# Optimization experiments

Measured on AMD Instinct MI355X. Metric: run time of the kernel, lower is better.

The kernel has to match this reference:

```python
import jax, jax.numpy as jnp
import numpy as np


def setup_inputs() -> dict:
    key = jax.random.key(0)
    ks = jax.random.split(key, 8)
    B, C, H, W = 4, 128, 64, 64
    d = C // 8
    return {
        "x": jax.random.normal(ks[0], (B, C, H, W), dtype=jnp.float32),
        "wq": jax.random.normal(ks[1], (d, C), dtype=jnp.float32) * 0.05,
        "bq": jax.random.normal(ks[2], (d,), dtype=jnp.float32) * 0.05,
        "wk": jax.random.normal(ks[3], (d, C), dtype=jnp.float32) * 0.05,
        "bk": jax.random.normal(ks[4], (d,), dtype=jnp.float32) * 0.05,
        "wv": jax.random.normal(ks[5], (C, C), dtype=jnp.float32) * 0.05,
        "bv": jax.random.normal(ks[6], (C,), dtype=jnp.float32) * 0.05,
        "gamma": jax.random.normal(ks[7], (1,), dtype=jnp.float32),
    }


def reference(x, wq, bq, wk, bk, wv, bv, gamma):
    B, C, H, W = x.shape
    N = H * W
    xf = x.reshape(B, C, N)                                  # [B,C,N]
    # 1x1 convs == per-pixel linear projections
    q = jnp.einsum('bcn,dc->bdn', xf, wq) + bq[None, :, None]  # [B,d,N]
    k = jnp.einsum('bcn,dc->bdn', xf, wk) + bk[None, :, None]  # [B,d,N]
    v = jnp.einsum('bcn,oc->bon', xf, wv) + bv[None, :, None]  # [B,C,N]
    scale = jnp.asarray(C, x.dtype) ** 0.5                     # note: scaled by sqrt(C), per source
    scores = jnp.einsum('bdn,bdm->bnm', q, k) / scale          # [B,N,N]
    attn = jax.nn.softmax(scores, axis=2)
    out = jnp.einsum('bcm,bnm->bcn', v, attn).reshape(B, C, H, W)
    return gamma[0] * out + x
```

## Files before the change

kernel.cpp:

```cpp
#include <hip/hip_runtime.h>
#include <hip/hip_bf16.h>
#include <math.h>

#define NB 4
#define NC 128
#define NN 4096
#define ND 16

typedef short s16x8 __attribute__((ext_vector_type(8)));
typedef float f32x4 __attribute__((ext_vector_type(4)));
typedef unsigned int u32;

extern "C" __device__ float __ocml_native_exp2_f32(float);

__device__ __forceinline__ unsigned short f2b(float f) {
    __hip_bfloat16 h = __float2bfloat16(f);
    return *reinterpret_cast<unsigned short*>(&h);
}
__device__ __forceinline__ u32 f2b2(float lo, float hi) {
    __hip_bfloat162 h2 = __float22bfloat162_rn(make_float2(lo, hi));
    return *reinterpret_cast<u32*>(&h2);
}
__device__ __forceinline__ void gll16(const unsigned short* src, unsigned short* ldsdst) {
    __builtin_amdgcn_global_load_lds((const __attribute__((address_space(1))) u32*)src,
                                     (__attribute__((address_space(3))) u32*)ldsdst, 16, 0, 0);
}

__global__ __launch_bounds__(256) void proj_kernel(
    const float* __restrict__ x,
    const float* __restrict__ wq, const float* __restrict__ bq,
    const float* __restrict__ wk, const float* __restrict__ bk,
    const float* __restrict__ wv, const float* __restrict__ bv,
    unsigned short* __restrict__ Qb, unsigned short* __restrict__ Kb,
    unsigned short* __restrict__ Vt)
{
    __shared__ unsigned short xsw[64 * 128];
    __shared__ unsigned short wsw[160 * 128];
    __shared__ float bl[160];

    const int t  = threadIdx.x;
    const int b  = blockIdx.x >> 6;
    const int n0 = (blockIdx.x & 63) << 6;

#pragma unroll
    for (int p = 0; p < 8; ++p) {
        const int idx = (p * 256 + t) * 4;
        const int c = idx >> 6, px0 = idx & 63;
        const float4 v4 = *(const float4*)&x[((size_t)(b * NC + c)) * NN + n0 + px0];
#pragma unroll
        for (int j = 0; j < 4; ++j) {
            const int px = px0 + j;
            xsw[px * 128 + (((c >> 3) ^ (px & 15)) << 3) + (c & 7)] = f2b((&v4.x)[j]);
        }
    }
#pragma unroll
    for (int p = 0; p < 20; ++p) {
        const int idx = (p * 256 + t) * 4;
        const int o = idx >> 7, c0 = idx & 127;
        const float* src = (o < 16) ? (wq + o * NC)
                         : (o < 32) ? (wk + (o - 16) * NC)
                                    : (wv + (o - 32) * NC);
        const float4 v4 = *(const float4*)&src[c0];
#pragma unroll
        for (int j = 0; j < 4; ++j) {
            const int c = c0 + j;
            wsw[o * 128 + (((c >> 3) ^ (o & 15)) << 3) + (c & 7)] = f2b((&v4.x)[j]);
        }
    }
    if (t < 160) bl[t] = (t < 16) ? bq[t] : (t < 32) ? bk[t - 16] : bv[t - 32];
    __syncthreads();

    const int lane = t & 63, w = t >> 6;
    const int l = lane & 15, h = lane >> 4;
    const int pxt = w;

    s16x8 af[4];
#pragma unroll
    for (int ks = 0; ks < 4; ++ks) {
        const int px = pxt * 16 + l;
        af[ks] = *(const s16x8*)&xsw[px * 128 + ((((ks * 4) + h) ^ (px & 15)) << 3)];
    }

    const float qscale = 1.4426950408889634f / sqrtf(128.0f);

#pragma unroll
    for (int ot = 0; ot < 10; ++ot) {
        f32x4 acc = (f32x4){0.f, 0.f, 0.f, 0.f};
        const int o = ot * 16 + l;
#pragma unroll
        for (int ks = 0; ks < 4; ++ks) {
            const s16x8 bf = *(const s16x8*)&wsw[o * 128 + ((((ks * 4) + h) ^ l) << 3)];
            acc = __builtin_amdgcn_mfma_f32_16x16x32_bf16(af[ks], bf, acc, 0, 0, 0);
        }
        const float bias = bl[o];
        if (ot == 0) {
#pragma unroll
            for (int r = 0; r < 4; ++r) {
                const int px = pxt * 16 + h * 4 + r;
                Qb[((size_t)b * NN + n0 + px) * ND + l] = f2b((acc[r] + bias) * qscale);
            }
        } else if (ot == 1) {
#pragma unroll
            for (int r = 0; r < 4; ++r) {
                const int px = pxt * 16 + h * 4 + r;
                Kb[((size_t)b * NN + n0 + px) * ND + l] = f2b(acc[r] + bias);
            }
        } else {
            const int c = ot * 16 + l - 32;
            uint2 pk;
            pk.x = f2b2(acc[0] + bias, acc[1] + bias);
            pk.y = f2b2(acc[2] + bias, acc[3] + bias);
            const int px0 = pxt * 16 + h * 4;
            *(uint2*)&Vt[((size_t)b * NC + c) * NN + n0 + px0] = pk;
        }
    }
}

__global__ __launch_bounds__(256) void attn_kernel(
    const unsigned short* __restrict__ Qb, const unsigned short* __restrict__ Kb,
    const unsigned short* __restrict__ Vt, const float* __restrict__ x,
    const float* __restrict__ gammap, float* __restrict__ out)
{
    __shared__ unsigned short vsw[2][128 * 64];
    __shared__ unsigned short ksh[2][64 * 24];
    __shared__ unsigned short psw[4][16 * 64];

    const int t    = threadIdx.x;
    const int lane = t & 63, w = t >> 6;
    const int l = lane & 15, h = lane >> 4;
    const int nt = w >> 1, ch = w & 1;

    const int bid = blockIdx.x;
    const int r_ = bid >> 8, s_ = bid & 255, xcd = s_ & 7, cu = s_ >> 3;
    const int b = xcd >> 1;
    const int tile = cu + ((xcd & 1) << 5) + (r_ << 6);
    const int n0 = tile << 5;

    s16x8 qf = {0, 0, 0, 0, 0, 0, 0, 0};
    if (h < 2) qf = *(const s16x8*)&Qb[((size_t)b * NN + n0 + nt * 16 + l) * ND + h * 8];

    const int vch = (lane & 7) ^ (lane >> 3);
    const int km = t >> 2, kp = t & 3;

    float mrun = -1e30f, lrun = 0.0f;
    f32x4 acc[4];
#pragma unroll
    for (int ct = 0; ct < 4; ++ct) acc[ct] = (f32x4){0.f, 0.f, 0.f, 0.f};

#pragma unroll
    for (int i = 0; i < 4; ++i) {
        const int c = w * 32 + i * 8 + (lane >> 3);
        gll16(&Vt[((size_t)b * NC + c) * NN + 0 + vch * 8],
              (unsigned short*)((char*)&vsw[0][0] + w * 4096 + i * 1024));
    }
    uint2 kreg = *(const uint2*)&Kb[((size_t)b * NN + 0 + km) * ND + kp * 4];
    *(uint2*)&ksh[0][km * 24 + kp * 4] = kreg;
    kreg = *(const uint2*)&Kb[((size_t)b * NN + 64 + km) * ND + kp * 4];
    __syncthreads();

    int cur = 0;
    for (int it = 0; it < 64; ++it) {
        const int m0n = ((it + 1) & 63) << 6;
#pragma unroll
        for (int i = 0; i < 4; ++i) {
            const int c = w * 32 + i * 8 + (lane >> 3);
            gll16(&Vt[((size_t)b * NC + c) * NN + m0n + vch * 8],
                  (unsigned short*)((char*)&vsw[cur ^ 1][0] + w * 4096 + i * 1024));
        }
        *(uint2*)&ksh[cur ^ 1][km * 24 + kp * 4] = kreg;
        kreg = *(const uint2*)&Kb[((size_t)b * NN + (((it + 2) & 63) << 6) + km) * ND + kp * 4];

        f32x4 sacc[4];
#pragma unroll
        for (int mt = 0; mt < 4; ++mt) {
            s16x8 afk = {0, 0, 0, 0, 0, 0, 0, 0};
            if (h < 2) afk = *(const s16x8*)&ksh[cur][(mt * 16 + l) * 24 + h * 8];
            sacc[mt] = __builtin_amdgcn_mfma_f32_16x16x32_bf16(
                afk, qf, (f32x4){0.f, 0.f, 0.f, 0.f}, 0, 0, 0);
        }

        float pmax = sacc[0][0];
#pragma unroll
        for (int mt = 0; mt < 4; ++mt)
#pragma unroll
            for (int r = 0; r < 4; ++r) pmax = fmaxf(pmax, sacc[mt][r]);
        pmax = fmaxf(pmax, __shfl_xor(pmax, 16));
        pmax = fmaxf(pmax, __shfl_xor(pmax, 32));
        const float mnew = fmaxf(mrun, pmax);
        const float rr = __ocml_native_exp2_f32(mrun - mnew);

        float p[4][4];
        float lsum = 0.0f;
#pragma unroll
        for (int mt = 0; mt < 4; ++mt)
#pragma unroll
            for (int r = 0; r < 4; ++r) {
                p[mt][r] = __ocml_native_exp2_f32(sacc[mt][r] - mnew);
                lsum += p[mt][r];
            }
        lsum += __shfl_xor(lsum, 16);
        lsum += __shfl_xor(lsum, 32);
        lrun = lrun * rr + lsum;
        mrun = mnew;

#pragma unroll
        for (int ct = 0; ct < 4; ++ct)
#pragma unroll
            for (int r = 0; r < 4; ++r) acc[ct][r] *= rr;

#pragma unroll
        for (int mt = 0; mt < 4; ++mt) {
            const int mch = mt * 2 + (h >> 1);
            const int base = l * 64 + ((mch ^ (l & 7)) << 3) + ((h & 1) << 2);
            *(u32*)&psw[w][base]     = f2b2(p[mt][0], p[mt][1]);
            *(u32*)&psw[w][base + 2] = f2b2(p[mt][2], p[mt][3]);
        }
        s16x8 pf[2];
#pragma unroll
        for (int kb = 0; kb < 2; ++kb)
            pf[kb] = *(const s16x8*)&psw[w][l * 64 + (((kb * 4 + h) ^ (l & 7)) << 3)];

#pragma unroll
        for (int ct = 0; ct < 4; ++ct) {
            const int c = ch * 64 + ct * 16 + l;
#pragma unroll
            for (int kb = 0; kb < 2; ++kb) {
                const s16x8 vf = *(const s16x8*)&vsw[cur][c * 64 + ((((kb * 4) + h) ^ (c & 7)) << 3)];
                acc[ct] = __builtin_amdgcn_mfma_f32_16x16x32_bf16(vf, pf[kb], acc[ct], 0, 0, 0);
            }
        }
        __syncthreads();
        cur ^= 1;
    }

    const float g = gammap[0];
    const float linv = 1.0f / lrun;
    const int n = n0 + nt * 16 + l;
#pragma unroll
    for (int ct = 0; ct < 4; ++ct)
#pragma unroll
        for (int r = 0; r < 4; ++r) {
            const int c = ch * 64 + ct * 16 + h * 4 + r;
            const size_t idx = ((size_t)b * NC + c) * NN + n;
            out[idx] = g * (acc[ct][r] * linv) + x[idx];
        }
}

extern "C" void kernel_launch(void* const* d_in, const int* in_sizes, int n_in,
                              void* d_out, int out_size, void* d_ws, size_t ws_size,
                              hipStream_t stream)
{
    const float* x  = (const float*)d_in[0];
    const float* wq = (const float*)d_in[1];
    const float* bq = (const float*)d_in[2];
    const float* wk = (const float*)d_in[3];
    const float* bk = (const float*)d_in[4];
    const float* wv = (const float*)d_in[5];
    const float* bv = (const float*)d_in[6];
    const float* gm = (const float*)d_in[7];
    float* out = (float*)d_out;

    unsigned short* Qb = (unsigned short*)d_ws;
    unsigned short* Kb = Qb + (size_t)NB * NN * ND;
    unsigned short* Vt = Kb + (size_t)NB * NN * ND;

    hipLaunchKernelGGL(proj_kernel, dim3(NB * 64), dim3(256), 0, stream,
                       x, wq, bq, wk, bk, wv, bv, Qb, Kb, Vt);
    hipLaunchKernelGGL(attn_kernel, dim3(512), dim3(256), 0, stream,
                       Qb, Kb, Vt, x, gm, out);
}
```

Before: 156.9 us.

## Rewrite attention with 32x32 MFMA, split-KV waves and LDS-free streaming

Adds a prep kernel that converts the weights to bf16 and folds the softmax scale into wq/bq. The projection kernel now reads x straight into registers, and V is stored in a 16-column tiled layout. The attention kernel moves to 32x32x16 MFMA and splits the KV range across wave pairs, merging their partial results through LDS at the end. Inside the loop it drops the LDS staging of K, V and P and passes P between lanes with shuffles instead. The goals are to cut LDS traffic and sync barriers and to raise MFMA efficiency, at the cost of uncoalesced direct global loads and an extra kernel launch.

```diff
diff --git a/kernel.cpp b/kernel.cpp
--- a/kernel.cpp
+++ b/kernel.cpp
@@ -5,10 +5,10 @@
 #define NB 4
 #define NC 128
 #define NN 4096
-#define ND 16
 
 typedef short s16x8 __attribute__((ext_vector_type(8)));
 typedef float f32x4 __attribute__((ext_vector_type(4)));
+typedef float f32x16 __attribute__((ext_vector_type(16)));
 typedef unsigned int u32;
 
 extern "C" __device__ float __ocml_native_exp2_f32(float);
@@ -21,229 +21,215 @@
     __hip_bfloat162 h2 = __float22bfloat162_rn(make_float2(lo, hi));
     return *reinterpret_cast<u32*>(&h2);
 }
-__device__ __forceinline__ void gll16(const unsigned short* src, unsigned short* ldsdst) {
-    __builtin_amdgcn_global_load_lds((const __attribute__((address_space(1))) u32*)src,
-                                     (__attribute__((address_space(3))) u32*)ldsdst, 16, 0, 0);
-}
-
-__global__ __launch_bounds__(256) void proj_kernel(
-    const float* __restrict__ x,
+
+__global__ __launch_bounds__(256) void prep_kernel(
     const float* __restrict__ wq, const float* __restrict__ bq,
     const float* __restrict__ wk, const float* __restrict__ bk,
     const float* __restrict__ wv, const float* __restrict__ bv,
+    unsigned short* __restrict__ Wb, float* __restrict__ Bf)
+{
+    const float s = 1.4426950408889634f / sqrtf(128.0f);
+    const int idx = blockIdx.x * 256 + threadIdx.x;
+    const int o = idx >> 7, c = idx & 127;
+    float v;
+    if (o < 16)      v = wq[o * 128 + c] * s;
+    else if (o < 32) v = wk[(o - 16) * 128 + c];
+    else             v = wv[(o - 32) * 128 + c];
+    Wb[o * 128 + c] = f2b(v);
+    if (blockIdx.x == 0 && threadIdx.x < 160) {
+        const int oo = threadIdx.x;
+        Bf[oo] = (oo < 16) ? bq[oo] * s : (oo < 32) ? bk[oo - 16] : bv[oo - 32];
+    }
+}
+
+__global__ __launch_bounds__(256, 2) void proj_kernel(
+    const float* __restrict__ x, const unsigned short* __restrict__ Wb,
+    const float* __restrict__ Bf,
     unsigned short* __restrict__ Qb, unsigned short* __restrict__ Kb,
-    unsigned short* __restrict__ Vt)
-{
-    __shared__ unsigned short xsw[64 * 128];
-    __shared__ unsigned short wsw[160 * 128];
-    __shared__ float bl[160];
-
-    const int t  = threadIdx.x;
-    const int b  = blockIdx.x >> 6;
-    const int n0 = (blockIdx.x & 63) << 6;
-
-#pragma unroll
-    for (int p = 0; p < 8; ++p) {
-        const int idx = (p * 256 + t) * 4;
-        const int c = idx >> 6, px0 = idx & 63;
-        const float4 v4 = *(const float4*)&x[((size_t)(b * NC + c)) * NN + n0 + px0];
-#pragma unroll
-        for (int j = 0; j < 4; ++j) {
-            const int px = px0 + j;
-            xsw[px * 128 + (((c >> 3) ^ (px & 15)) << 3) + (c & 7)] = f2b((&v4.x)[j]);
-        }
-    }
-#pragma unroll
-    for (int p = 0; p < 20; ++p) {
-        const int idx = (p * 256 + t) * 4;
-        const int o = idx >> 7, c0 = idx & 127;
-        const float* src = (o < 16) ? (wq + o * NC)
-                         : (o < 32) ? (wk + (o - 16) * NC)
-                                    : (wv + (o - 32) * NC);
-        const float4 v4 = *(const float4*)&src[c0];
-#pragma unroll
-        for (int j = 0; j < 4; ++j) {
-            const int c = c0 + j;
-            wsw[o * 128 + (((c >> 3) ^ (o & 15)) << 3) + (c & 7)] = f2b((&v4.x)[j]);
-        }
-    }
-    if (t < 160) bl[t] = (t < 16) ? bq[t] : (t < 32) ? bk[t - 16] : bv[t - 32];
-    __syncthreads();
-
+    unsigned short* __restrict__ V2)
+{
+    const int t = threadIdx.x;
     const int lane = t & 63, w = t >> 6;
     const int l = lane & 15, h = lane >> 4;
-    const int pxt = w;
-
-    s16x8 af[4];
+    const int pxt = w & 1, oh = w >> 1;
+    const int b = blockIdx.x >> 7;
+    const int n0 = (blockIdx.x & 127) * 32;
+    const int n = n0 + pxt * 16 + l;
+
+    s16x8 bx[4];
 #pragma unroll
     for (int ks = 0; ks < 4; ++ks) {
-        const int px = pxt * 16 + l;
-        af[ks] = *(const s16x8*)&xsw[px * 128 + ((((ks * 4) + h) ^ (px & 15)) << 3)];
-    }
-
-    const float qscale = 1.4426950408889634f / sqrtf(128.0f);
-
-#pragma unroll
-    for (int ot = 0; ot < 10; ++ot) {
+        float xv[8];
+#pragma unroll
+        for (int j = 0; j < 8; ++j)
+            xv[j] = x[((size_t)(b * 128 + ks * 32 + h * 8 + j)) * 4096 + n];
+        u32* pw = (u32*)&bx[ks];
+        pw[0] = f2b2(xv[0], xv[1]);
+        pw[1] = f2b2(xv[2], xv[3]);
+        pw[2] = f2b2(xv[4], xv[5]);
+        pw[3] = f2b2(xv[6], xv[7]);
+    }
+
+#pragma unroll
+    for (int i = 0; i < 5; ++i) {
+        const int ot = oh * 5 + i;
+        const int o0 = ot * 16;
         f32x4 acc = (f32x4){0.f, 0.f, 0.f, 0.f};
-        const int o = ot * 16 + l;
 #pragma unroll
         for (int ks = 0; ks < 4; ++ks) {
-            const s16x8 bf = *(const s16x8*)&wsw[o * 128 + ((((ks * 4) + h) ^ l) << 3)];
-            acc = __builtin_amdgcn_mfma_f32_16x16x32_bf16(af[ks], bf, acc, 0, 0, 0);
-        }
-        const float bias = bl[o];
+            const s16x8 wf = *(const s16x8*)&Wb[(o0 + l) * 128 + ks * 32 + h * 8];
+            acc = __builtin_amdgcn_mfma_f32_16x16x32_bf16(wf, bx[ks], acc, 0, 0, 0);
+        }
+        const float r0 = acc[0] + Bf[o0 + h * 4 + 0];
+        const float r1 = acc[1] + Bf[o0 + h * 4 + 1];
+        const float r2 = acc[2] + Bf[o0 + h * 4 + 2];
+        const float r3 = acc[3] + Bf[o0 + h * 4 + 3];
         if (ot == 0) {
-#pragma unroll
-            for (int r = 0; r < 4; ++r) {
-                const int px = pxt * 16 + h * 4 + r;
-                Qb[((size_t)b * NN + n0 + px) * ND + l] = f2b((acc[r] + bias) * qscale);
-            }
+            uint2 pk_; pk_.x = f2b2(r0, r1); pk_.y = f2b2(r2, r3);
+            *(uint2*)&Qb[((size_t)b * 4096 + n) * 16 + h * 4] = pk_;
         } else if (ot == 1) {
-#pragma unroll
-            for (int r = 0; r < 4; ++r) {
-                const int px = pxt * 16 + h * 4 + r;
-                Kb[((size_t)b * NN + n0 + px) * ND + l] = f2b(acc[r] + bias);
-            }
+            uint2 pk_; pk_.x = f2b2(r0, r1); pk_.y = f2b2(r2, r3);
+            *(uint2*)&Kb[((size_t)b * 4096 + n) * 16 + h * 4] = pk_;
         } else {
-            const int c = ot * 16 + l - 32;
-            uint2 pk;
-            pk.x = f2b2(acc[0] + bias, acc[1] + bias);
-            pk.y = f2b2(acc[2] + bias, acc[3] + bias);
-            const int px0 = pxt * 16 + h * 4;
-            *(uint2*)&Vt[((size_t)b * NC + c) * NN + n0 + px0] = pk;
-        }
-    }
-}
-
-__global__ __launch_bounds__(256) void attn_kernel(
+            const int c0 = (ot - 2) * 16 + h * 4;
+            const size_t base = ((size_t)(b * 256 + (n >> 4))) * 128 * 16 + (n & 15);
+            V2[base + (size_t)(c0 + 0) * 16] = f2b(r0);
+            V2[base + (size_t)(c0 + 1) * 16] = f2b(r1);
+            V2[base + (size_t)(c0 + 2) * 16] = f2b(r2);
+            V2[base + (size_t)(c0 + 3) * 16] = f2b(r3);
+        }
+    }
+}
+
+__global__ __launch_bounds__(256, 2) void attn_kernel(
     const unsigned short* __restrict__ Qb, const unsigned short* __restrict__ Kb,
-    const unsigned short* __restrict__ Vt, const float* __restrict__ x,
+    const unsigned short* __restrict__ V2, const float* __restrict__ x,
     const float* __restrict__ gammap, float* __restrict__ out)
 {
-    __shared__ unsigned short vsw[2][128 * 64];
-    __shared__ unsigned short ksh[2][64 * 24];
-    __shared__ unsigned short psw[4][16 * 64];
-
-    const int t    = threadIdx.x;
+    __shared__ float mlsM[2][32], mlsL[2][32];
+    __shared__ float buf[2][64][36];
+
+    const int t = threadIdx.x;
     const int lane = t & 63, w = t >> 6;
-    const int l = lane & 15, h = lane >> 4;
-    const int nt = w >> 1, ch = w & 1;
+    const int ch = w & 1, kvs = w >> 1;
+    const int n31 = lane & 31, h5 = lane >> 5;
 
     const int bid = blockIdx.x;
-    const int r_ = bid >> 8, s_ = bid & 255, xcd = s_ & 7, cu = s_ >> 3;
+    const int xcd = bid & 7;
     const int b = xcd >> 1;
-    const int tile = cu + ((xcd & 1) << 5) + (r_ << 6);
-    const int n0 = tile << 5;
-
-    s16x8 qf = {0, 0, 0, 0, 0, 0, 0, 0};
-    if (h < 2) qf = *(const s16x8*)&Qb[((size_t)b * NN + n0 + nt * 16 + l) * ND + h * 8];
-
-    const int vch = (lane & 7) ^ (lane >> 3);
-    const int km = t >> 2, kp = t & 3;
+    const int qt = ((bid >> 3) << 1) | (xcd & 1);
+    const int n = qt * 32 + n31;
+
+    const s16x8 qf = *(const s16x8*)&Qb[((size_t)b * 4096 + n) * 16 + h5 * 8];
+
+    f32x16 z16;
+#pragma unroll
+    for (int r = 0; r < 16; ++r) z16[r] = 0.0f;
 
     float mrun = -1e30f, lrun = 0.0f;
-    f32x4 acc[4];
-#pragma unroll
-    for (int ct = 0; ct < 4; ++ct) acc[ct] = (f32x4){0.f, 0.f, 0.f, 0.f};
-
-#pragma unroll
-    for (int i = 0; i < 4; ++i) {
-        const int c = w * 32 + i * 8 + (lane >> 3);
-        gll16(&Vt[((size_t)b * NC + c) * NN + 0 + vch * 8],
-              (unsigned short*)((char*)&vsw[0][0] + w * 4096 + i * 1024));
-    }
-    uint2 kreg = *(const uint2*)&Kb[((size_t)b * NN + 0 + km) * ND + kp * 4];
-    *(uint2*)&ksh[0][km * 24 + kp * 4] = kreg;
-    kreg = *(const uint2*)&Kb[((size_t)b * NN + 64 + km) * ND + kp * 4];
-    __syncthreads();
-
-    int cur = 0;
-    for (int it = 0; it < 64; ++it) {
-        const int m0n = ((it + 1) & 63) << 6;
-#pragma unroll
-        for (int i = 0; i < 4; ++i) {
-            const int c = w * 32 + i * 8 + (lane >> 3);
-            gll16(&Vt[((size_t)b * NC + c) * NN + m0n + vch * 8],
-                  (unsigned short*)((char*)&vsw[cur ^ 1][0] + w * 4096 + i * 1024));
-        }
-        *(uint2*)&ksh[cur ^ 1][km * 24 + kp * 4] = kreg;
-        kreg = *(const uint2*)&Kb[((size_t)b * NN + (((it + 2) & 63) << 6) + km) * ND + kp * 4];
-
-        f32x4 sacc[4];
-#pragma unroll
-        for (int mt = 0; mt < 4; ++mt) {
-            s16x8 afk = {0, 0, 0, 0, 0, 0, 0, 0};
-            if (h < 2) afk = *(const s16x8*)&ksh[cur][(mt * 16 + l) * 24 + h * 8];
-            sacc[mt] = __builtin_amdgcn_mfma_f32_16x16x32_bf16(
-                afk, qf, (f32x4){0.f, 0.f, 0.f, 0.f}, 0, 0, 0);
-        }
-
-        float pmax = sacc[0][0];
-#pragma unroll
-        for (int mt = 0; mt < 4; ++mt)
-#pragma unroll
-            for (int r = 0; r < 4; ++r) pmax = fmaxf(pmax, sacc[mt][r]);
-        pmax = fmaxf(pmax, __shfl_xor(pmax, 16));
-        pmax = fmaxf(pmax, __shfl_xor(pmax, 32));
+    f32x16 acc0 = z16, acc1 = z16;
+
+    const unsigned short* Kbb = Kb + (size_t)b * 4096 * 16;
+    const unsigned short* Vbb = V2 + (size_t)b * 256 * 128 * 16;
+
+    for (int step = 0; step < 32; ++step) {
+        const int m0 = kvs * 2048 + step * 64;
+
+        s16x8 vf[4][2];
+#pragma unroll
+        for (int kb = 0; kb < 4; ++kb) {
+            const size_t vt = (size_t)((m0 >> 4) + kb) * 128 * 16;
+            vf[kb][0] = *(const s16x8*)&Vbb[vt + (size_t)(ch * 64 + n31) * 16 + h5 * 8];
+            vf[kb][1] = *(const s16x8*)&Vbb[vt + (size_t)(ch * 64 + 32 + n31) * 16 + h5 * 8];
+        }
+        const s16x8 kf0 = *(const s16x8*)&Kbb[(size_t)(m0 + n31) * 16 + h5 * 8];
+        const s16x8 kf1 = *(const s16x8*)&Kbb[(size_t)(m0 + 32 + n31) * 16 + h5 * 8];
+        f32x16 s0 = __builtin_amdgcn_mfma_f32_32x32x16_bf16(kf0, qf, z16, 0, 0, 0);
+        f32x16 s1 = __builtin_amdgcn_mfma_f32_32x32x16_bf16(kf1, qf, z16, 0, 0, 0);
+
+        float mx[8];
+#pragma unroll
+        for (int r = 0; r < 8; ++r)
+            mx[r] = fmaxf(fmaxf(s0[r], s0[r + 8]), fmaxf(s1[r], s1[r + 8]));
+#pragma unroll
+        for (int d = 4; d > 0; d >>= 1)
+#pragma unroll
+            for (int r = 0; r < d; ++r) mx[r] = fmaxf(mx[r], mx[r + d]);
+        const float pmax = fmaxf(mx[0], __shfl_xor(mx[0], 32));
         const float mnew = fmaxf(mrun, pmax);
         const float rr = __ocml_native_exp2_f32(mrun - mnew);
-
-        float p[4][4];
-        float lsum = 0.0f;
-#pragma unroll
-        for (int mt = 0; mt < 4; ++mt)
-#pragma unroll
-            for (int r = 0; r < 4; ++r) {
-                p[mt][r] = __ocml_native_exp2_f32(sacc[mt][r] - mnew);
-                lsum += p[mt][r];
-            }
-        lsum += __shfl_xor(lsum, 16);
+        float lsum = 0.f;
+#pragma unroll
+        for (int r = 0; r < 16; ++r) {
+            s0[r] = __ocml_native_exp2_f32(s0[r] - mnew); lsum += s0[r];
+            s1[r] = __ocml_native_exp2_f32(s1[r] - mnew); lsum += s1[r];
+        }
         lsum += __shfl_xor(lsum, 32);
         lrun = lrun * rr + lsum;
         mrun = mnew;
-
-#pragma unroll
-        for (int ct = 0; ct < 4; ++ct)
-#pragma unroll
-            for (int r = 0; r < 4; ++r) acc[ct][r] *= rr;
-
-#pragma unroll
-        for (int mt = 0; mt < 4; ++mt) {
-            const int mch = mt * 2 + (h >> 1);
-            const int base = l * 64 + ((mch ^ (l & 7)) << 3) + ((h & 1) << 2);
-            *(u32*)&psw[w][base]     = f2b2(p[mt][0], p[mt][1]);
-            *(u32*)&psw[w][base + 2] = f2b2(p[mt][2], p[mt][3]);
-        }
-        s16x8 pf[2];
-#pragma unroll
-        for (int kb = 0; kb < 2; ++kb)
-            pf[kb] = *(const s16x8*)&psw[w][l * 64 + (((kb * 4 + h) ^ (l & 7)) << 3)];
-
-#pragma unroll
-        for (int ct = 0; ct < 4; ++ct) {
-            const int c = ch * 64 + ct * 16 + l;
-#pragma unroll
-            for (int kb = 0; kb < 2; ++kb) {
-                const s16x8 vf = *(const s16x8*)&vsw[cur][c * 64 + ((((kb * 4) + h) ^ (c & 7)) << 3)];
-                acc[ct] = __builtin_amdgcn_mfma_f32_16x16x32_bf16(vf, pf[kb], acc[ct], 0, 0, 0);
+#pragma unroll
+        for (int r = 0; r < 16; ++r) { acc0[r] *= rr; acc1[r] *= rr; }
+
+        u32 q2[16], x2[16];
+#pragma unroll
+        for (int i = 0; i < 8; ++i) {
+            q2[i]     = f2b2(s0[2 * i], s0[2 * i + 1]);
+            q2[8 + i] = f2b2(s1[2 * i], s1[2 * i + 1]);
+        }
+#pragma unroll
+        for (int i = 0; i < 16; ++i)
+            x2[i] = (u32)__shfl_xor((int)q2[i], 32);
+
+#pragma unroll
+        for (int kb = 0; kb < 4; ++kb) {
+            const int base = (kb >> 1) * 8 + (kb & 1) * 4;
+            s16x8 pf;
+            u32* pw = (u32*)&pf;
+            pw[0] = h5 ? x2[base + 2] : q2[base + 0];
+            pw[1] = h5 ? x2[base + 3] : q2[base + 1];
+            pw[2] = h5 ? q2[base + 2] : x2[base + 0];
+            pw[3] = h5 ? q2[base + 3] : x2[base + 1];
+            acc0 = __builtin_amdgcn_mfma_f32_32x32x16_bf16(vf[kb][0], pf, acc0, 0, 0, 0);
+            acc1 = __builtin_amdgcn_mfma_f32_32x32x16_bf16(vf[kb][1], pf, acc1, 0, 0, 0);
+        }
+    }
+
+    if (ch == 0 && h5 == 0) { mlsM[kvs][n31] = mrun; mlsL[kvs][n31] = lrun; }
+    __syncthreads();
+    const float ma = mlsM[0][n31], mb = mlsM[1][n31];
+    const float mg = fmaxf(ma, mb);
+    const float lg = __ocml_native_exp2_f32(ma - mg) * mlsL[0][n31]
+                   + __ocml_native_exp2_f32(mb - mg) * mlsL[1][n31];
+    const float sc = __ocml_native_exp2_f32(mrun - mg);
+#pragma unroll
+    for (int r = 0; r < 16; ++r) { acc0[r] *= sc; acc1[r] *= sc; }
+
+    if (kvs == 1) {
+#pragma unroll
+        for (int r = 0; r < 16; ++r) {
+            buf[ch][lane][r]      = acc0[r];
+            buf[ch][lane][16 + r] = acc1[r];
+        }
+    }
+    __syncthreads();
+    if (kvs == 0) {
+        const float g = gammap[0];
+        const float inv = 1.0f / lg;
+#pragma unroll
+        for (int r = 0; r < 16; ++r) {
+            acc0[r] += buf[ch][lane][r];
+            acc1[r] += buf[ch][lane][16 + r];
+        }
+#pragma unroll
+        for (int ct = 0; ct < 2; ++ct)
+#pragma unroll
+            for (int r = 0; r < 16; ++r) {
+                const int c = ch * 64 + ct * 32 + (r & 3) + 8 * (r >> 2) + 4 * h5;
+                const size_t idx = ((size_t)b * 128 + c) * 4096 + n;
+                const float v = (ct == 0) ? acc0[r] : acc1[r];
+                out[idx] = g * (v * inv) + x[idx];
             }
-        }
-        __syncthreads();
-        cur ^= 1;
-    }
-
-    const float g = gammap[0];
-    const float linv = 1.0f / lrun;
-    const int n = n0 + nt * 16 + l;
-#pragma unroll
-    for (int ct = 0; ct < 4; ++ct)
-#pragma unroll
-        for (int r = 0; r < 4; ++r) {
-            const int c = ch * 64 + ct * 16 + h * 4 + r;
-            const size_t idx = ((size_t)b * NC + c) * NN + n;
-            out[idx] = g * (acc[ct][r] * linv) + x[idx];
-        }
+    }
 }
 
 extern "C" void kernel_launch(void* const* d_in, const int* in_sizes, int n_in,
@@ -260,12 +246,16 @@
     const float* gm = (const float*)d_in[7];
     float* out = (float*)d_out;
 
-    unsigned short* Qb = (unsigned short*)d_ws;
-    unsigned short* Kb = Qb + (size_t)NB * NN * ND;
-    unsigned short* Vt = Kb + (size_t)NB * NN * ND;
-
-    hipLaunchKernelGGL(proj_kernel, dim3(NB * 64), dim3(256), 0, stream,
-                       x, wq, bq, wk, bk, wv, bv, Qb, Kb, Vt);
+    unsigned short* Wb = (unsigned short*)d_ws;
+    float*          Bf = (float*)((char*)d_ws + 40960);
+    unsigned short* Qb = (unsigned short*)((char*)d_ws + 41600);
+    unsigned short* Kb = Qb + (size_t)NB * NN * 16;
+    unsigned short* V2 = Kb + (size_t)NB * NN * 16;
+
+    hipLaunchKernelGGL(prep_kernel, dim3(80), dim3(256), 0, stream,
+                       wq, bq, wk, bk, wv, bv, Wb, Bf);
+    hipLaunchKernelGGL(proj_kernel, dim3(512), dim3(256), 0, stream,
+                       x, Wb, Bf, Qb, Kb, V2);
     hipLaunchKernelGGL(attn_kernel, dim3(512), dim3(256), 0, stream,
-                       Qb, Kb, Vt, x, gm, out);
-}
+                       Qb, Kb, V2, x, gm, out);
+}
```

After: 170.0 us. +8.4%, slower.
